# Performance work log

Hardware: AMD Instinct MI355X
Metric: run time of the kernel (lower is better)

## Reference

```python
import jax, jax.numpy as jnp
import numpy as np

# Fixed architecture constants from AlgelogicNetwork.__init__
M, J, I, L, W = 4, 2, 3, 2, 9
B = 1048576  # batch size (only free dim)


def setup_inputs() -> dict:
    key = jax.random.key(0)
    ks = jax.random.split(key, 7)
    state = jax.random.normal(ks[0], (B, W * L), dtype=jnp.float32)
    # rule.constants ~ U(-1, 1), rule.gammas ~ U(0, 1), stacked over M rules
    constants = jax.random.uniform(ks[1], (M, J, L), minval=-1.0, maxval=1.0, dtype=jnp.float32)
    gammas = jax.random.uniform(ks[2], (M, J, L), dtype=jnp.float32)
    # body Linears (L -> I), one per (rule m, premise j); head Linear (I -> L) per rule
    W_body = jax.random.normal(ks[3], (M, J, I, L), dtype=jnp.float32) * 0.5
    b_body = jax.random.normal(ks[4], (M, J, I), dtype=jnp.float32) * 0.1
    W_head = jax.random.normal(ks[5], (M, L, I), dtype=jnp.float32) * 0.5
    b_head = jax.random.normal(ks[6], (M, L), dtype=jnp.float32) * 0.1
    return {
        "state": state,
        "constants": constants,
        "gammas": gammas,
        "W_body": W_body,
        "b_body": b_body,
        "W_head": W_head,
        "b_head": b_head,
    }


def reference(state, constants, gammas, W_body, b_body, W_head, b_head):
    s = state.reshape(-1, W, L)                       # [B, W, L]
    g = jnp.clip(gammas, 0.0, 1.0)                    # sigmoid() in source = clamp; [M, J, L]
    wgt = 1.0 - g                                     # [M, J, L]

    # match_scores[m,j,b,w] = sum_l (1-g[m,j,l]) * (const[m,j,l] - s[b,w,l])^2
    # L=2 fixed: unroll over l to avoid a [M,J,B,W,L] intermediate
    ms = sum(
        wgt[:, :, l, None, None]
        * (constants[:, :, l, None, None] - s[None, None, :, :, l]) ** 2
        for l in range(L)
    )                                                  # [M, J, B, W]

    attn = jax.nn.softmax(-ms, axis=-1)                # softmax over W positions (temperature=1)
    best = jnp.einsum('mjbw,bwl->mjbl', attn, s)       # soft-gathered propositions
    match_quality = jnp.sum(attn * ms, axis=-1).sum(axis=1)   # [M, B], summed over premises j

    captured = jnp.einsum('mjbl,mjil->mjbi', best, W_body) + b_body[:, :, None, :]  # body Linear
    g_avg = g.mean(axis=-1)                            # [M, J]
    captured_vars = jnp.einsum('mj,mjbi->mbi', g_avg, captured)                     # [M, B, I]

    rule_out = jnp.einsum('mbi,mli->mbl', captured_vars, W_head) + b_head[:, None, :]  # [M, B, L]

    # similarity[m,b,w] = -sum_l (rule_out[m,b,l] - s[b,w,l])^2
    sim = -jnp.sum((rule_out[:, :, None, :] - s[None]) ** 2, axis=-1)  # [M, B, W]
    confidence = jnp.exp(-match_quality)               # [M, B]
    return jnp.einsum('mb,mbw->bw', confidence, sim)   # [B, W]
```

## Files before the change

kernel.cpp:

```cpp
#include <hip/hip_runtime.h>

namespace {
constexpr int kM = 4, kJ = 2, kI = 3, kL = 2, kW = 9;
constexpr float kInvLn2 = 1.4426950408889634f;

typedef float v2f __attribute__((ext_vector_type(2)));

__device__ __forceinline__ float fexp2(float x) { return __builtin_amdgcn_exp2f(x); }

__global__ __launch_bounds__(256, 4) void algelogic_one(
    const float* __restrict__ state,
    const float* __restrict__ constants,
    const float* __restrict__ gammas,
    const float* __restrict__ W_body,
    const float* __restrict__ b_body,
    const float* __restrict__ W_head,
    const float* __restrict__ b_head,
    float* __restrict__ out) {
  __shared__ float sdp[72];
  const int t = threadIdx.x;
  const int b = blockIdx.x * 256 + t;

  const float2* sr = reinterpret_cast<const float2*>(state) + (size_t)b * kW;
  v2f s[kW];
#pragma unroll
  for (int w = 0; w < kW; ++w) {
    const float2 v = sr[w];
    v2f x; x.x = v.x; x.y = v.y;
    s[w] = x;
  }

  if (t < 8) {
    const int mj = t, m = t >> 1, j = t & 1;
    const float g0 = fminf(fmaxf(gammas[mj * kL + 0], 0.f), 1.f);
    const float g1 = fminf(fmaxf(gammas[mj * kL + 1], 0.f), 1.f);
    const float w0 = 1.f - g0, w1 = 1.f - g1;
    const float c0 = constants[mj * kL + 0], c1 = constants[mj * kL + 1];
    const float gavg = 0.5f * (g0 + g1);
    float* base = sdp + m * 16;
    base[0 * 2 + j] = c0;
    base[1 * 2 + j] = c1;
    base[2 * 2 + j] = -w0 * kInvLn2;
    base[3 * 2 + j] = -w1 * kInvLn2;
#pragma unroll
    for (int l = 0; l < kL; ++l)
#pragma unroll
      for (int lp = 0; lp < kL; ++lp) {
        float acc = 0.f;
#pragma unroll
        for (int i = 0; i < kI; ++i)
          acc += W_head[(m * kL + l) * kI + i] * W_body[(mj * kI + i) * kL + lp];
        base[(4 + l * kL + lp) * 2 + j] = gavg * acc;
      }
  } else if (t >= 64 && t < 68) {
    const int m = t - 64;
#pragma unroll
    for (int l = 0; l < kL; ++l) {
      float d = b_head[m * kL + l];
#pragma unroll
      for (int j = 0; j < kJ; ++j) {
        const int mj = m * kJ + j;
        const float g0 = fminf(fmaxf(gammas[mj * kL + 0], 0.f), 1.f);
        const float g1 = fminf(fmaxf(gammas[mj * kL + 1], 0.f), 1.f);
        const float gavg = 0.5f * (g0 + g1);
        float acc = 0.f;
#pragma unroll
        for (int i = 0; i < kI; ++i)
          acc += W_head[(m * kL + l) * kI + i] * b_body[mj * kI + i];
        d += gavg * acc;
      }
      sdp[64 + m * kL + l] = d;
    }
  }
  __syncthreads();

  float Cs = 0.f, X0 = 0.f, X1 = 0.f, K = 0.f;
#pragma unroll
  for (int m = 0; m < kM; ++m) {
    const float* P = sdp + m * 16;
    v2f c0;  c0.x = P[0];  c0.y = P[1];
    v2f c1;  c1.x = P[2];  c1.y = P[3];
    v2f w0n; w0n.x = P[4]; w0n.y = P[5];
    v2f w1n; w1n.x = P[6]; w1n.y = P[7];

    v2f psum = {1e-35f, 1e-35f};
    v2f pb0 = {0.f, 0.f}, pb1 = {0.f, 0.f}, pmq = {0.f, 0.f};
#pragma unroll
    for (int w = 0; w < kW; ++w) {
      const float sx = s[w].x, sy = s[w].y;
      const v2f d0 = sx - c0;
      const v2f d1 = sy - c1;
      v2f msN = (d0 * d0) * w0n;
      msN += (d1 * d1) * w1n;
      v2f e; e.x = fexp2(msN.x); e.y = fexp2(msN.y);
      psum += e;
      pb0 += e * sx;
      pb1 += e * sy;
      pmq += e * msN;
    }

    v2f rinv;
    rinv.x = __builtin_amdgcn_rcpf(psum.x);
    rinv.y = __builtin_amdgcn_rcpf(psum.y);
    const v2f bb0 = pb0 * rinv, bb1 = pb1 * rinv;
    const v2f mqv = pmq * rinv;
    const float conf = fexp2(mqv.x + mqv.y);

    v2f C00; C00.x = P[8];  C00.y = P[9];
    v2f C01; C01.x = P[10]; C01.y = P[11];
    v2f C10; C10.x = P[12]; C10.y = P[13];
    v2f C11; C11.x = P[14]; C11.y = P[15];
    const v2f t0 = C00 * bb0 + C01 * bb1;
    const v2f t1 = C10 * bb0 + C11 * bb1;
    const float r0 = sdp[64 + m * 2 + 0] + t0.x + t0.y;
    const float r1 = sdp[64 + m * 2 + 1] + t1.x + t1.y;

    Cs += conf;
    X0 = fmaf(conf, r0, X0);
    X1 = fmaf(conf, r1, X1);
    K = fmaf(conf, fmaf(r0, r0, r1 * r1), K);
  }

  const float X02 = 2.f * X0, X12 = 2.f * X1;
  float* orow = out + (size_t)b * kW;
#pragma unroll
  for (int w = 0; w < kW; ++w) {
    const v2f q = s[w] * s[w];
    orow[w] = fmaf(X02, s[w].x, fmaf(X12, s[w].y, fmaf(-Cs, q.x + q.y, -K)));
  }
}
}

extern "C" void kernel_launch(void* const* d_in, const int* in_sizes, int n_in,
                              void* d_out, int out_size, void* d_ws, size_t ws_size,
                              hipStream_t stream) {
  const float* state     = (const float*)d_in[0];
  const float* constants = (const float*)d_in[1];
  const float* gammas    = (const float*)d_in[2];
  const float* W_body    = (const float*)d_in[3];
  const float* b_body    = (const float*)d_in[4];
  const float* W_head    = (const float*)d_in[5];
  const float* b_head    = (const float*)d_in[6];
  float* out = (float*)d_out;

  const int B = in_sizes[0] / (kW * kL);
  hipLaunchKernelGGL(algelogic_one, dim3(B / 256), dim3(256), 0, stream,
                     state, constants, gammas, W_body, b_body, W_head, b_head, out);
}
```

Before: 32.10 us.

## Split rule loop across thread pairs and combine partial sums via shuffle

Each batch row is now handled by two adjacent threads, each computing two of the four rules, and their partial accumulators are combined with a lane shuffle. The output row is split between the pair (five and four columns). This doubles thread count and halves per-thread exp/ALU work to improve latency hiding. In exchange each state row is loaded twice, and the stores become less contiguous per thread.

```diff
diff --git a/kernel.cpp b/kernel.cpp
--- a/kernel.cpp
+++ b/kernel.cpp
@@ -8,7 +8,7 @@
 
 __device__ __forceinline__ float fexp2(float x) { return __builtin_amdgcn_exp2f(x); }
 
-__global__ __launch_bounds__(256, 4) void algelogic_one(
+__global__ __launch_bounds__(256, 4) void algelogic_msplit(
     const float* __restrict__ state,
     const float* __restrict__ constants,
     const float* __restrict__ gammas,
@@ -19,9 +19,10 @@
     float* __restrict__ out) {
   __shared__ float sdp[72];
   const int t = threadIdx.x;
-  const int b = blockIdx.x * 256 + t;
+  const int sub = t & 1;
+  const size_t e = (size_t)blockIdx.x * 128 + (t >> 1);
 
-  const float2* sr = reinterpret_cast<const float2*>(state) + (size_t)b * kW;
+  const float2* sr = reinterpret_cast<const float2*>(state) + e * kW;
   v2f s[kW];
 #pragma unroll
   for (int w = 0; w < kW; ++w) {
@@ -76,7 +77,8 @@
 
   float Cs = 0.f, X0 = 0.f, X1 = 0.f, K = 0.f;
 #pragma unroll
-  for (int m = 0; m < kM; ++m) {
+  for (int mi = 0; mi < 2; ++mi) {
+    const int m = sub * 2 + mi;
     const float* P = sdp + m * 16;
     v2f c0;  c0.x = P[0];  c0.y = P[1];
     v2f c1;  c1.x = P[2];  c1.y = P[3];
@@ -92,11 +94,11 @@
       const v2f d1 = sy - c1;
       v2f msN = (d0 * d0) * w0n;
       msN += (d1 * d1) * w1n;
-      v2f e; e.x = fexp2(msN.x); e.y = fexp2(msN.y);
-      psum += e;
-      pb0 += e * sx;
-      pb1 += e * sy;
-      pmq += e * msN;
+      v2f ev; ev.x = fexp2(msN.x); ev.y = fexp2(msN.y);
+      psum += ev;
+      pb0 += ev * sx;
+      pb1 += ev * sy;
+      pmq += ev * msN;
     }
 
     v2f rinv;
@@ -121,12 +123,21 @@
     K = fmaf(conf, fmaf(r0, r0, r1 * r1), K);
   }
 
+  Cs += __shfl_xor(Cs, 1, 64);
+  X0 += __shfl_xor(X0, 1, 64);
+  X1 += __shfl_xor(X1, 1, 64);
+  K  += __shfl_xor(K, 1, 64);
+
   const float X02 = 2.f * X0, X12 = 2.f * X1;
-  float* orow = out + (size_t)b * kW;
+  float* orow = out + e * kW;
+  const int wlo = sub ? 5 : 0;
+  const int whi = sub ? 9 : 5;
 #pragma unroll
   for (int w = 0; w < kW; ++w) {
-    const v2f q = s[w] * s[w];
-    orow[w] = fmaf(X02, s[w].x, fmaf(X12, s[w].y, fmaf(-Cs, q.x + q.y, -K)));
+    if (w >= wlo && w < whi) {
+      const v2f q = s[w] * s[w];
+      orow[w] = fmaf(X02, s[w].x, fmaf(X12, s[w].y, fmaf(-Cs, q.x + q.y, -K)));
+    }
   }
 }
 }
@@ -144,6 +155,6 @@
   float* out = (float*)d_out;
 
   const int B = in_sizes[0] / (kW * kL);
-  hipLaunchKernelGGL(algelogic_one, dim3(B / 256), dim3(256), 0, stream,
+  hipLaunchKernelGGL(algelogic_msplit, dim3(B / 128), dim3(256), 0, stream,
                      state, constants, gammas, W_body, b_body, W_head, b_head, out);
 }
```

Result: slower. 33.28 us (+3.7%).
